# Kernel tuning notes

Hardware: AMD Instinct MI355X
Metric: run time of the kernel (lower is better)

Reference implementation:

```python
import jax, jax.numpy as jnp
import numpy as np

EMBED = 1024
HEADS = 16
HEAD_DIM = EMBED // HEADS


def setup_inputs() -> dict:
    key = jax.random.key(0)
    ks = jax.random.split(key, 5)
    s = 0.02
    x = jax.random.normal(ks[0], (2, 2048, EMBED), dtype=jnp.float32)
    W_qkv = jax.random.normal(ks[1], (EMBED, 3 * EMBED), dtype=jnp.float32) * s
    b_qkv = jnp.zeros((3 * EMBED,), dtype=jnp.float32)
    W_proj = jax.random.normal(ks[2], (EMBED, EMBED), dtype=jnp.float32) * s
    b_proj = jnp.zeros((EMBED,), dtype=jnp.float32)
    return {"x": x, "W_qkv": W_qkv, "b_qkv": b_qkv, "W_proj": W_proj, "b_proj": b_proj}


def reference(x, W_qkv, b_qkv, W_proj, b_proj):
    B, N, _ = x.shape
    scale = HEAD_DIM ** -0.5
    qkv = x @ W_qkv + b_qkv                     # [B,N,3E]
    qkv = qkv.reshape(B, N, 3, HEADS, HEAD_DIM)
    q = qkv[:, :, 0].transpose(0, 2, 1, 3) * scale  # [B,H,N,D]
    k = qkv[:, :, 1].transpose(0, 2, 1, 3)
    v = qkv[:, :, 2].transpose(0, 2, 1, 3)
    attn = jnp.einsum('bhnd,bhmd->bhnm', q, k)  # [B,H,N,N]
    attn = jax.nn.softmax(attn, axis=-1)
    out = jnp.einsum('bhnm,bhmd->bhnd', attn, v)  # [B,H,N,D]
    out = out.transpose(0, 2, 1, 3).reshape(B, N, HEADS * HEAD_DIM)
    return out @ W_proj + b_proj
```

## Files before the change

### kernel.cpp

```cpp
#include <hip/hip_runtime.h>
#include <hip/hip_bf16.h>
#include <stdint.h>

typedef unsigned short u16;
typedef __bf16 bf16x8 __attribute__((ext_vector_type(8)));
typedef float f32x4 __attribute__((ext_vector_type(4)));
typedef float f32x16 __attribute__((ext_vector_type(16)));

__device__ __forceinline__ u16 f2bf(float f) {
    union { float f; unsigned u; } x; x.f = f;
    unsigned u = x.u;
    u += 0x7FFFu + ((u >> 16) & 1u);
    return (u16)(u >> 16);
}
__device__ __forceinline__ float bf2f(u16 h) {
    union { unsigned u; float f; } x; x.u = ((unsigned)h) << 16; return x.f;
}

typedef __attribute__((address_space(1))) void gvoid;
typedef __attribute__((address_space(3))) void lvoid;
__device__ __forceinline__ void gl2lds16(const void* g, void* l) {
    __builtin_amdgcn_global_load_lds((gvoid*)g, (lvoid*)l, 16, 0, 0);
}

__global__ __launch_bounds__(256) void prep_kernel(
    const float* __restrict__ x, u16* __restrict__ xb,
    const float* __restrict__ Wqkv, u16* __restrict__ wqkvT,
    const float* __restrict__ Wproj, u16* __restrict__ wprojT)
{
    __shared__ u16 tile[64][65];
    const int blk = blockIdx.x;
    const int tid = threadIdx.x;

    if (blk < 2048) {
        const size_t i = ((size_t)blk * 256 + tid) * 8;
        float4 a = *(const float4*)(x + i);
        float4 b = *(const float4*)(x + i + 4);
        ushort4 oa, ob;
        oa.x = f2bf(a.x); oa.y = f2bf(a.y); oa.z = f2bf(a.z); oa.w = f2bf(a.w);
        ob.x = f2bf(b.x); ob.y = f2bf(b.y); ob.z = f2bf(b.z); ob.w = f2bf(b.w);
        *(ushort4*)(xb + i) = oa;
        *(ushort4*)(xb + i + 4) = ob;
        return;
    }
    const float* in; u16* out; int rows, cols, bx, by;
    if (blk < 2816) { int t = blk - 2048; in = Wqkv;  out = wqkvT;  rows = 1024; cols = 3072; bx = t % 48; by = t / 48; }
    else            { int t = blk - 2816; in = Wproj; out = wprojT; rows = 1024; cols = 1024; bx = t % 16; by = t / 16; }
#pragma unroll
    for (int i = 0; i < 16; i++) {
        int e = i * 256 + tid;
        int r = e >> 6, c = e & 63;
        tile[r][c] = f2bf(in[(size_t)(by * 64 + r) * cols + bx * 64 + c]);
    }
    __syncthreads();
#pragma unroll
    for (int i = 0; i < 16; i++) {
        int e = i * 256 + tid;
        int r = e >> 6, c = e & 63;
        out[(size_t)(bx * 64 + r) * rows + by * 64 + c] = tile[c][r];
    }
}

__global__ __launch_bounds__(256) void gemm_qkv(
    const u16* __restrict__ A, const u16* __restrict__ Bt,
    const float* __restrict__ bias,
    u16* __restrict__ q, u16* __restrict__ ko, u16* __restrict__ vt)
{
    constexpr int K = 1024;
    __shared__ __align__(16) u16 smem[64 * 64 + 128 * 64];
    u16* sA = smem;
    u16* sB = smem + 4096;
    const int tid = threadIdx.x;
    const int wave = tid >> 6, lane = tid & 63;
    const int quad = lane >> 4, l16 = lane & 15;
    const int wm = (wave >> 1) * 32, wn = (wave & 1) * 64;
    const int m0 = blockIdx.y * 64, n0 = blockIdx.x * 128;
    const int srow = lane >> 3;
    const int scolz = ((lane & 7) ^ srow) * 8;

    f32x4 acc[2][4];
#pragma unroll
    for (int i = 0; i < 2; i++)
#pragma unroll
        for (int j = 0; j < 4; j++)
#pragma unroll
            for (int r = 0; r < 4; r++) acc[i][j][r] = 0.f;

    for (int kt = 0; kt < K; kt += 64) {
        __syncthreads();
#pragma unroll
        for (int t = 0; t < 2; t++) {
            int rb = wave * 16 + t * 8;
            gl2lds16(A + (size_t)(m0 + rb + srow) * K + kt + scolz, &sA[rb * 64]);
        }
#pragma unroll
        for (int t = 0; t < 4; t++) {
            int rb = wave * 32 + t * 8;
            gl2lds16(Bt + (size_t)(n0 + rb + srow) * K + kt + scolz, &sB[rb * 64]);
        }
        __syncthreads();
#pragma unroll
        for (int kk = 0; kk < 64; kk += 32) {
            bf16x8 af[2], bfr[4];
            int sl = (((kk >> 3) + quad) ^ (l16 & 7)) * 8;
#pragma unroll
            for (int t = 0; t < 2; t++)
                af[t] = *(const bf16x8*)&sA[(wm + t * 16 + l16) * 64 + sl];
#pragma unroll
            for (int t = 0; t < 4; t++)
                bfr[t] = *(const bf16x8*)&sB[(wn + t * 16 + l16) * 64 + sl];
#pragma unroll
            for (int i = 0; i < 2; i++)
#pragma unroll
                for (int j = 0; j < 4; j++)
                    acc[i][j] = __builtin_amdgcn_mfma_f32_16x16x32_bf16(
                        af[i], bfr[j], acc[i][j], 0, 0, 0);
        }
    }

    const float QSCALE = 0.18033688011112042f;
    const float sc = (n0 < 1024) ? QSCALE : 1.0f;
    __syncthreads();
#pragma unroll
    for (int i = 0; i < 2; i++) {
#pragma unroll
        for (int j = 0; j < 4; j++) {
            float bv = bias[n0 + wn + j * 16 + l16];
#pragma unroll
            for (int r = 0; r < 4; r++) {
                float v = (acc[i][j][r] + bv) * sc;
                smem[(wm + i * 16 + quad * 4 + r) * 132 + wn + j * 16 + l16] = f2bf(v);
            }
        }
    }
    __syncthreads();

    if (n0 < 2048) {
        u16* dst = (n0 < 1024) ? q : ko;
#pragma unroll
        for (int it = 0; it < 4; it++) {
            int c = it * 256 + tid;
            int m_l = c >> 4;
            int n8 = (c & 15) * 8;
            uint4 w = *(const uint4*)&smem[m_l * 132 + n8];
            int n = n0 + n8;
            int h = (n & 1023) >> 6, d = n & 63;
            int m = m0 + m_l;
            int b = m >> 11, t = m & 2047;
            *(uint4*)(dst + ((size_t)(b * 16 + h) * 2048 + t) * 64 + d) = w;
        }
    } else {
        constexpr int PERM[16] = {0,1,2,3, 8,9,10,11, 4,5,6,7, 12,13,14,15};
        int nv = n0 - 2048;
        int n_l = tid & 127, mh = tid >> 7;
        int hh = (nv >> 6) + (n_l >> 6);
        int d = n_l & 63;
        int bb = m0 >> 11, t0 = m0 & 2047;
        u16* vrow = vt + ((size_t)(bb * 16 + hh) * 64 + d) * 2048 + t0 + mh * 32;
#pragma unroll
        for (int it = 0; it < 4; it++) {
            int base = mh * 32 + it * 8;
            union { u16 s[8]; uint4 w; } pk;
#pragma unroll
            for (int i = 0; i < 8; i++) {
                int pos = base + i;
                int row = (pos & ~15) | PERM[pos & 15];
                pk.s[i] = smem[row * 132 + n_l];
            }
            *(uint4*)(vrow + it * 8) = pk.w;
        }
    }
}

__global__ __launch_bounds__(256, 4) void attn_kernel(
    const u16* __restrict__ q, const u16* __restrict__ ko,
    const u16* __restrict__ vt,
    u16* __restrict__ op0, u16* __restrict__ op1,
    float* __restrict__ lp0, float* __restrict__ lp1)
{
    __shared__ __align__(16) u16 sK[2][64 * 72];
    __shared__ __align__(16) u16 sV[2][64 * 72];

    const int tid = threadIdx.x;
    const int wave = tid >> 6, lane = tid & 63;
    const int l31 = lane & 31, hi = lane >> 5;

    const int lid = blockIdx.x;
    const int xcd = lid & 7, idx = lid >> 3;
    const int h = xcd * 2 + (idx & 1);
    const int b = (idx >> 1) & 1;
    const int q0 = ((idx >> 2) & 15) * 128;
    const int khalf = idx >> 6;
    const int kbase = khalf * 1024;
    const size_t bh = (size_t)(b * 16 + h);

    const u16* qp  = q  + bh * 2048 * 64;
    const u16* kp  = ko + bh * 2048 * 64;
    const u16* vtp = vt + bh * 64 * 2048;

    bf16x8 qf[4];
    {
        const u16* qrow = qp + (size_t)(q0 + wave * 32 + l31) * 64 + hi * 8;
#pragma unroll
        for (int d = 0; d < 4; d++)
            qf[d] = *(const bf16x8*)(qrow + d * 16);
    }

    const int sr0 = tid >> 3;
    const int sc0 = (tid & 7) * 8;
    const int sr1 = sr0 + 32;

    uint4 pk0 = *(const uint4*)(kp + (size_t)(kbase + sr0) * 64 + sc0);
    uint4 pk1 = *(const uint4*)(kp + (size_t)(kbase + sr1) * 64 + sc0);
    uint4 pv0 = *(const uint4*)(vtp + (size_t)sr0 * 2048 + kbase + sc0);
    uint4 pv1 = *(const uint4*)(vtp + (size_t)sr1 * 2048 + kbase + sc0);

    f32x16 accO[2];
#pragma unroll
    for (int d = 0; d < 2; d++)
#pragma unroll
        for (int r = 0; r < 16; r++) accO[d][r] = 0.f;
    float ls[4] = {0.f, 0.f, 0.f, 0.f};

    for (int t = 0; t < 16; ++t) {
        const int cur = t & 1;
        u16* sKc = &sK[cur][0];
        u16* sVc = &sV[cur][0];
        *(uint4*)&sKc[sr0 * 72 + sc0] = pk0;
        *(uint4*)&sKc[sr1 * 72 + sc0] = pk1;
        *(uint4*)&sVc[sr0 * 72 + sc0] = pv0;
        *(uint4*)&sVc[sr1 * 72 + sc0] = pv1;
        if (t < 15) {
            int nt = kbase + (t + 1) * 64;
            pk0 = *(const uint4*)(kp + (size_t)(nt + sr0) * 64 + sc0);
            pk1 = *(const uint4*)(kp + (size_t)(nt + sr1) * 64 + sc0);
            pv0 = *(const uint4*)(vtp + (size_t)sr0 * 2048 + nt + sc0);
            pv1 = *(const uint4*)(vtp + (size_t)sr1 * 2048 + nt + sc0);
        }
        __syncthreads();

#pragma unroll
        for (int rb = 0; rb < 2; rb++) {
            f32x16 S;
#pragma unroll
            for (int r = 0; r < 16; r++) S[r] = 0.f;
            const u16* krd = &sKc[(rb * 32 + l31) * 72 + hi * 8];
#pragma unroll
            for (int d = 0; d < 4; d++) {
                bf16x8 kf = *(const bf16x8*)(krd + d * 16);
                S = __builtin_amdgcn_mfma_f32_32x32x16_bf16(kf, qf[d], S, 0, 0, 0);
            }
            union { float f; unsigned u; } e[16];
#pragma unroll
            for (int r = 0; r < 16; r++) {
                e[r].f = __builtin_amdgcn_exp2f(S[r]);
                ls[r & 3] += e[r].f;
            }
#pragma unroll
            for (int ks2 = 0; ks2 < 2; ks2++) {
                union { unsigned u[4]; bf16x8 v; } pa;
#pragma unroll
                for (int s = 0; s < 4; s++) {
                    unsigned r0 = e[ks2 * 8 + 2 * s].u + 0x8000u;
                    unsigned r1 = e[ks2 * 8 + 2 * s + 1].u + 0x8000u;
                    pa.u[s] = (r1 & 0xFFFF0000u) | (r0 >> 16);
                }
                const int nb = rb * 32 + ks2 * 16 + hi * 8;
#pragma unroll
                for (int db = 0; db < 2; db++) {
                    bf16x8 vf = *(const bf16x8*)&sVc[(db * 32 + l31) * 72 + nb];
                    accO[db] = __builtin_amdgcn_mfma_f32_32x32x16_bf16(pa.v, vf, accO[db], 0, 0, 0);
                }
            }
        }
    }

    u16* op = khalf ? op1 : op0;
    float* lp = khalf ? lp1 : lp0;

    float lsum = (ls[0] + ls[1]) + (ls[2] + ls[3]);
    float ltot = lsum + __shfl_xor(lsum, 32, 64);
    int qq0 = q0 + wave * 32;
    if (hi == 0) lp[bh * 2048 + qq0 + l31] = ltot;

#pragma unroll
    for (int db = 0; db < 2; db++)
#pragma unroll
        for (int r = 0; r < 16; r++) {
            int tq = qq0 + (r & 3) + 8 * (r >> 2) + 4 * hi;
            size_t row = (size_t)b * 2048 + tq;
            op[row * 1024 + h * 64 + db * 32 + l31] = f2bf(accO[db][r]);
        }
}

__global__ __launch_bounds__(256) void combine_kernel(
    const u16* __restrict__ op0, const u16* __restrict__ op1,
    const float* __restrict__ lp0, const float* __restrict__ lp1,
    u16* __restrict__ ob)
{
    const size_t i = ((size_t)blockIdx.x * 256 + threadIdx.x) * 8;
    int m = (int)(i >> 10), e = (int)(i & 1023);
    int b = m >> 11, t = m & 2047, h = e >> 6;
    float inv = 1.f / (lp0[(size_t)(b * 16 + h) * 2048 + t] +
                       lp1[(size_t)(b * 16 + h) * 2048 + t]);
    union { uint4 w; u16 s[8]; } a, c, o;
    a.w = *(const uint4*)(op0 + i);
    c.w = *(const uint4*)(op1 + i);
#pragma unroll
    for (int k = 0; k < 8; k++)
        o.s[k] = f2bf((bf2f(a.s[k]) + bf2f(c.s[k])) * inv);
    *(uint4*)(ob + i) = o.w;
}

__global__ __launch_bounds__(256) void gemm_proj(
    const u16* __restrict__ A, const u16* __restrict__ Bt,
    const float* __restrict__ bias, float* __restrict__ out)
{
    constexpr int K = 1024;
    __shared__ __align__(16) u16 sA[64 * 64];
    __shared__ __align__(16) u16 sB[128 * 64];
    const int tid = threadIdx.x;
    const int wave = tid >> 6, lane = tid & 63;
    const int quad = lane >> 4, l16 = lane & 15;
    const int wm = (wave & 1) * 32, wn = (wave >> 1) * 64;

    const int lid = blockIdx.x;
    const int xcd = lid & 7, idx = lid >> 3;
    const int m0 = (xcd * 8 + (idx & 7)) * 64;
    const int n0 = (idx >> 3) * 128;

    const int srow = lane >> 3;
    const int scolz = ((lane & 7) ^ srow) * 8;

    f32x4 acc[2][4];
#pragma unroll
    for (int i = 0; i < 2; i++)
#pragma unroll
        for (int j = 0; j < 4; j++)
#pragma unroll
            for (int r = 0; r < 4; r++) acc[i][j][r] = 0.f;

    for (int kt = 0; kt < K; kt += 64) {
        __syncthreads();
#pragma unroll
        for (int t = 0; t < 2; t++) {
            int rb = wave * 16 + t * 8;
            gl2lds16(A + (size_t)(m0 + rb + srow) * K + kt + scolz, &sA[rb * 64]);
        }
#pragma unroll
        for (int t = 0; t < 4; t++) {
            int rb = wave * 32 + t * 8;
            gl2lds16(Bt + (size_t)(n0 + rb + srow) * K + kt + scolz, &sB[rb * 64]);
        }
        __syncthreads();
#pragma unroll
        for (int kk = 0; kk < 64; kk += 32) {
            bf16x8 af[2], bfr[4];
            int sl = (((kk >> 3) + quad) ^ (l16 & 7)) * 8;
#pragma unroll
            for (int t = 0; t < 2; t++)
                af[t] = *(const bf16x8*)&sA[(wm + t * 16 + l16) * 64 + sl];
#pragma unroll
            for (int t = 0; t < 4; t++)
                bfr[t] = *(const bf16x8*)&sB[(wn + t * 16 + l16) * 64 + sl];
#pragma unroll
            for (int i = 0; i < 2; i++)
#pragma unroll
                for (int j = 0; j < 4; j++)
                    acc[i][j] = __builtin_amdgcn_mfma_f32_16x16x32_bf16(
                        af[i], bfr[j], acc[i][j], 0, 0, 0);
        }
    }

#pragma unroll
    for (int i = 0; i < 2; i++) {
#pragma unroll
        for (int j = 0; j < 4; j++) {
            int n = n0 + wn + j * 16 + l16;
            float bv = bias[n];
#pragma unroll
            for (int r = 0; r < 4; r++) {
                int m = m0 + wm + i * 16 + quad * 4 + r;
                out[(size_t)m * 1024 + n] = acc[i][j][r] + bv;
            }
        }
    }
}

extern "C" void kernel_launch(void* const* d_in, const int* in_sizes, int n_in,
                              void* d_out, int out_size, void* d_ws, size_t ws_size,
                              hipStream_t stream) {
    const float* x     = (const float*)d_in[0];
    const float* Wqkv  = (const float*)d_in[1];
    const float* bqkv  = (const float*)d_in[2];
    const float* Wproj = (const float*)d_in[3];
    const float* bproj = (const float*)d_in[4];
    float* out = (float*)d_out;
    char* ws = (char*)d_ws;

    u16* wqkvT  = (u16*)(ws);
    u16* wprojT = (u16*)(ws +  6291456);
    u16* xb     = (u16*)(ws +  8388608);
    u16* qb     = (u16*)(ws + 16777216);
    u16* kb     = (u16*)(ws + 25165824);
    u16* vtb    = (u16*)(ws + 33554432);
    u16* ob     = (u16*)(ws + 41943040);

    u16*   op0 = ob;
    u16*   op1 = xb;
    float* lp0 = (float*)wqkvT;
    float* lp1 = (float*)(ws + 262144);

    prep_kernel<<<dim3(3072), 256, 0, stream>>>(x, xb, Wqkv, wqkvT, Wproj, wprojT);
    gemm_qkv<<<dim3(24, 64), 256, 0, stream>>>(xb, wqkvT, bqkv, qb, kb, vtb);
    attn_kernel<<<dim3(1024), 256, 0, stream>>>(qb, kb, vtb, op0, op1, lp0, lp1);
    combine_kernel<<<dim3(2048), 256, 0, stream>>>(op0, op1, lp0, lp1, ob);
    gemm_proj<<<dim3(512), 256, 0, stream>>>(ob, wprojT, bproj, out);
}
```

Measured before the change: 189.6 us.

## Merge attention key-split halves in-block and shrink projection GEMM tiles

The attention kernel now runs both key halves inside one 512-thread block, with waves 4-7 taking the second half. The partial outputs and row sums are combined through shared memory, which removes the separate combine kernel and its global round trip of partial outputs. Separately, the projection GEMM moves to 32x128 tiles with twice as many blocks, to improve occupancy and tail balance. The trade-offs are fewer, larger attention blocks with double the LDS per block, and less data reuse per projection tile.

```diff
diff --git a/kernel.cpp b/kernel.cpp
--- a/kernel.cpp
+++ b/kernel.cpp
@@ -172,26 +172,24 @@
     }
 }
 
-__global__ __launch_bounds__(256, 4) void attn_kernel(
+__global__ __launch_bounds__(512) void attn_kernel(
     const u16* __restrict__ q, const u16* __restrict__ ko,
-    const u16* __restrict__ vt,
-    u16* __restrict__ op0, u16* __restrict__ op1,
-    float* __restrict__ lp0, float* __restrict__ lp1)
+    const u16* __restrict__ vt, u16* __restrict__ ob)
 {
-    __shared__ __align__(16) u16 sK[2][64 * 72];
-    __shared__ __align__(16) u16 sV[2][64 * 72];
+    __shared__ __align__(16) u16 sK[2][2][64 * 72];
+    __shared__ __align__(16) u16 sV[2][2][64 * 72];
 
     const int tid = threadIdx.x;
     const int wave = tid >> 6, lane = tid & 63;
     const int l31 = lane & 31, hi = lane >> 5;
+    const int khalf = wave >> 2, qw = wave & 3;
+    const int kbase = khalf * 1024;
 
     const int lid = blockIdx.x;
     const int xcd = lid & 7, idx = lid >> 3;
     const int h = xcd * 2 + (idx & 1);
     const int b = (idx >> 1) & 1;
     const int q0 = ((idx >> 2) & 15) * 128;
-    const int khalf = idx >> 6;
-    const int kbase = khalf * 1024;
     const size_t bh = (size_t)(b * 16 + h);
 
     const u16* qp  = q  + bh * 2048 * 64;
@@ -200,14 +198,15 @@
 
     bf16x8 qf[4];
     {
-        const u16* qrow = qp + (size_t)(q0 + wave * 32 + l31) * 64 + hi * 8;
+        const u16* qrow = qp + (size_t)(q0 + qw * 32 + l31) * 64 + hi * 8;
 #pragma unroll
         for (int d = 0; d < 4; d++)
             qf[d] = *(const bf16x8*)(qrow + d * 16);
     }
 
-    const int sr0 = tid >> 3;
-    const int sc0 = (tid & 7) * 8;
+    const int gt = tid & 255;
+    const int sr0 = gt >> 3;
+    const int sc0 = (gt & 7) * 8;
     const int sr1 = sr0 + 32;
 
     uint4 pk0 = *(const uint4*)(kp + (size_t)(kbase + sr0) * 64 + sc0);
@@ -224,8 +223,8 @@
 
     for (int t = 0; t < 16; ++t) {
         const int cur = t & 1;
-        u16* sKc = &sK[cur][0];
-        u16* sVc = &sV[cur][0];
+        u16* sKc = &sK[khalf][cur][0];
+        u16* sVc = &sV[khalf][cur][0];
         *(uint4*)&sKc[sr0 * 72 + sc0] = pk0;
         *(uint4*)&sKc[sr1 * 72 + sc0] = pk1;
         *(uint4*)&sVc[sr0 * 72 + sc0] = pv0;
@@ -275,41 +274,36 @@
         }
     }
 
-    u16* op = khalf ? op1 : op0;
-    float* lp = khalf ? lp1 : lp0;
-
     float lsum = (ls[0] + ls[1]) + (ls[2] + ls[3]);
     float ltot = lsum + __shfl_xor(lsum, 32, 64);
-    int qq0 = q0 + wave * 32;
-    if (hi == 0) lp[bh * 2048 + qq0 + l31] = ltot;
-
-#pragma unroll
-    for (int db = 0; db < 2; db++)
-#pragma unroll
-        for (int r = 0; r < 16; r++) {
-            int tq = qq0 + (r & 3) + 8 * (r >> 2) + 4 * hi;
-            size_t row = (size_t)b * 2048 + tq;
-            op[row * 1024 + h * 64 + db * 32 + l31] = f2bf(accO[db][r]);
-        }
-}
-
-__global__ __launch_bounds__(256) void combine_kernel(
-    const u16* __restrict__ op0, const u16* __restrict__ op1,
-    const float* __restrict__ lp0, const float* __restrict__ lp1,
-    u16* __restrict__ ob)
-{
-    const size_t i = ((size_t)blockIdx.x * 256 + threadIdx.x) * 8;
-    int m = (int)(i >> 10), e = (int)(i & 1023);
-    int b = m >> 11, t = m & 2047, h = e >> 6;
-    float inv = 1.f / (lp0[(size_t)(b * 16 + h) * 2048 + t] +
-                       lp1[(size_t)(b * 16 + h) * 2048 + t]);
-    union { uint4 w; u16 s[8]; } a, c, o;
-    a.w = *(const uint4*)(op0 + i);
-    c.w = *(const uint4*)(op1 + i);
-#pragma unroll
-    for (int k = 0; k < 8; k++)
-        o.s[k] = f2bf((bf2f(a.s[k]) + bf2f(c.s[k])) * inv);
-    *(uint4*)(ob + i) = o.w;
+
+    float* xO = (float*)&sK[0][0][0];
+    float* xL = (float*)&sV[0][0][0];
+
+    __syncthreads();
+    if (hi == 0) xL[khalf * 128 + qw * 32 + l31] = ltot;
+    if (khalf == 1) {
+#pragma unroll
+        for (int db = 0; db < 2; db++)
+#pragma unroll
+            for (int r = 0; r < 16; r++) {
+                int rloc = (r & 3) + 8 * (r >> 2) + 4 * hi;
+                xO[(qw * 32 + rloc) * 64 + db * 32 + l31] = accO[db][r];
+            }
+    }
+    __syncthreads();
+    if (khalf == 0) {
+#pragma unroll
+        for (int db = 0; db < 2; db++)
+#pragma unroll
+            for (int r = 0; r < 16; r++) {
+                int rloc = (r & 3) + 8 * (r >> 2) + 4 * hi;
+                float inv = 1.f / (xL[qw * 32 + rloc] + xL[128 + qw * 32 + rloc]);
+                float v = (accO[db][r] + xO[(qw * 32 + rloc) * 64 + db * 32 + l31]) * inv;
+                int tq = q0 + qw * 32 + rloc;
+                ob[((size_t)b * 2048 + tq) * 1024 + h * 64 + db * 32 + l31] = f2bf(v);
+            }
+    }
 }
 
 __global__ __launch_bounds__(256) void gemm_proj(
@@ -317,34 +311,33 @@
     const float* __restrict__ bias, float* __restrict__ out)
 {
     constexpr int K = 1024;
-    __shared__ __align__(16) u16 sA[64 * 64];
+    __shared__ __align__(16) u16 sA[32 * 64];
     __shared__ __align__(16) u16 sB[128 * 64];
     const int tid = threadIdx.x;
     const int wave = tid >> 6, lane = tid & 63;
     const int quad = lane >> 4, l16 = lane & 15;
-    const int wm = (wave & 1) * 32, wn = (wave >> 1) * 64;
+    const int wn = wave * 32;
 
     const int lid = blockIdx.x;
     const int xcd = lid & 7, idx = lid >> 3;
-    const int m0 = (xcd * 8 + (idx & 7)) * 64;
-    const int n0 = (idx >> 3) * 128;
+    const int m0 = (xcd * 16 + (idx & 15)) * 32;
+    const int n0 = (idx >> 4) * 128;
 
     const int srow = lane >> 3;
     const int scolz = ((lane & 7) ^ srow) * 8;
 
-    f32x4 acc[2][4];
+    f32x4 acc[2][2];
 #pragma unroll
     for (int i = 0; i < 2; i++)
 #pragma unroll
-        for (int j = 0; j < 4; j++)
+        for (int j = 0; j < 2; j++)
 #pragma unroll
             for (int r = 0; r < 4; r++) acc[i][j][r] = 0.f;
 
     for (int kt = 0; kt < K; kt += 64) {
         __syncthreads();
-#pragma unroll
-        for (int t = 0; t < 2; t++) {
-            int rb = wave * 16 + t * 8;
+        {
+            int rb = wave * 8;
             gl2lds16(A + (size_t)(m0 + rb + srow) * K + kt + scolz, &sA[rb * 64]);
         }
 #pragma unroll
@@ -355,18 +348,18 @@
         __syncthreads();
 #pragma unroll
         for (int kk = 0; kk < 64; kk += 32) {
-            bf16x8 af[2], bfr[4];
+            bf16x8 af[2], bfr[2];
             int sl = (((kk >> 3) + quad) ^ (l16 & 7)) * 8;
 #pragma unroll
             for (int t = 0; t < 2; t++)
-                af[t] = *(const bf16x8*)&sA[(wm + t * 16 + l16) * 64 + sl];
-#pragma unroll
-            for (int t = 0; t < 4; t++)
+                af[t] = *(const bf16x8*)&sA[(t * 16 + l16) * 64 + sl];
+#pragma unroll
+            for (int t = 0; t < 2; t++)
                 bfr[t] = *(const bf16x8*)&sB[(wn + t * 16 + l16) * 64 + sl];
 #pragma unroll
             for (int i = 0; i < 2; i++)
 #pragma unroll
-                for (int j = 0; j < 4; j++)
+                for (int j = 0; j < 2; j++)
                     acc[i][j] = __builtin_amdgcn_mfma_f32_16x16x32_bf16(
                         af[i], bfr[j], acc[i][j], 0, 0, 0);
         }
@@ -375,12 +368,12 @@
 #pragma unroll
     for (int i = 0; i < 2; i++) {
 #pragma unroll
-        for (int j = 0; j < 4; j++) {
+        for (int j = 0; j < 2; j++) {
             int n = n0 + wn + j * 16 + l16;
             float bv = bias[n];
 #pragma unroll
             for (int r = 0; r < 4; r++) {
-                int m = m0 + wm + i * 16 + quad * 4 + r;
+                int m = m0 + i * 16 + quad * 4 + r;
                 out[(size_t)m * 1024 + n] = acc[i][j][r] + bv;
             }
         }
@@ -406,14 +399,8 @@
     u16* vtb    = (u16*)(ws + 33554432);
     u16* ob     = (u16*)(ws + 41943040);
 
-    u16*   op0 = ob;
-    u16*   op1 = xb;
-    float* lp0 = (float*)wqkvT;
-    float* lp1 = (float*)(ws + 262144);
-
     prep_kernel<<<dim3(3072), 256, 0, stream>>>(x, xb, Wqkv, wqkvT, Wproj, wprojT);
     gemm_qkv<<<dim3(24, 64), 256, 0, stream>>>(xb, wqkvT, bqkv, qb, kb, vtb);
-    attn_kernel<<<dim3(1024), 256, 0, stream>>>(qb, kb, vtb, op0, op1, lp0, lp1);
-    combine_kernel<<<dim3(2048), 256, 0, stream>>>(op0, op1, lp0, lp1, ob);
-    gemm_proj<<<dim3(512), 256, 0, stream>>>(ob, wprojT, bproj, out);
-}
+    attn_kernel<<<dim3(512), 512, 0, stream>>>(qb, kb, vtb, ob);
+    gemm_proj<<<dim3(1024), 256, 0, stream>>>(ob, wprojT, bproj, out);
+}
```

New measurement: 178.8 us. -5.7%, faster.

## Fuse split-K attention combine into projection GEMM A-tile load

Applied to the files above, without the earlier changes.

Removes the separate combine kernel. The projection GEMM now loads both partial attention outputs and their row sums directly, normalizes them, and writes the bf16 result into shared memory as its A tile. This avoids writing and re-reading the combined intermediate buffer and saves one kernel launch. In exchange the A load becomes a synchronous register path instead of a direct global-to-LDS load, the normalization is redone for every N-block, and the block tile is shrunk to 32 rows with twice as many blocks, which lowers data reuse per block.

```diff
diff --git a/kernel.cpp b/kernel.cpp
--- a/kernel.cpp
+++ b/kernel.cpp
@@ -293,59 +293,53 @@
         }
 }
 
-__global__ __launch_bounds__(256) void combine_kernel(
+__global__ __launch_bounds__(256) void gemm_proj(
     const u16* __restrict__ op0, const u16* __restrict__ op1,
     const float* __restrict__ lp0, const float* __restrict__ lp1,
-    u16* __restrict__ ob)
-{
-    const size_t i = ((size_t)blockIdx.x * 256 + threadIdx.x) * 8;
-    int m = (int)(i >> 10), e = (int)(i & 1023);
-    int b = m >> 11, t = m & 2047, h = e >> 6;
-    float inv = 1.f / (lp0[(size_t)(b * 16 + h) * 2048 + t] +
-                       lp1[(size_t)(b * 16 + h) * 2048 + t]);
-    union { uint4 w; u16 s[8]; } a, c, o;
-    a.w = *(const uint4*)(op0 + i);
-    c.w = *(const uint4*)(op1 + i);
-#pragma unroll
-    for (int k = 0; k < 8; k++)
-        o.s[k] = f2bf((bf2f(a.s[k]) + bf2f(c.s[k])) * inv);
-    *(uint4*)(ob + i) = o.w;
-}
-
-__global__ __launch_bounds__(256) void gemm_proj(
-    const u16* __restrict__ A, const u16* __restrict__ Bt,
+    const u16* __restrict__ Bt,
     const float* __restrict__ bias, float* __restrict__ out)
 {
     constexpr int K = 1024;
-    __shared__ __align__(16) u16 sA[64 * 64];
+    __shared__ __align__(16) u16 sA[32 * 64];
     __shared__ __align__(16) u16 sB[128 * 64];
     const int tid = threadIdx.x;
     const int wave = tid >> 6, lane = tid & 63;
     const int quad = lane >> 4, l16 = lane & 15;
-    const int wm = (wave & 1) * 32, wn = (wave >> 1) * 64;
+    const int wn = wave * 32;
 
     const int lid = blockIdx.x;
     const int xcd = lid & 7, idx = lid >> 3;
-    const int m0 = (xcd * 8 + (idx & 7)) * 64;
-    const int n0 = (idx >> 3) * 128;
+    const int m0 = (xcd * 16 + (idx & 15)) * 32;
+    const int n0 = (idx >> 4) * 128;
 
     const int srow = lane >> 3;
     const int scolz = ((lane & 7) ^ srow) * 8;
 
-    f32x4 acc[2][4];
+    f32x4 acc[2][2];
 #pragma unroll
     for (int i = 0; i < 2; i++)
 #pragma unroll
-        for (int j = 0; j < 4; j++)
+        for (int j = 0; j < 2; j++)
 #pragma unroll
             for (int r = 0; r < 4; r++) acc[i][j][r] = 0.f;
 
     for (int kt = 0; kt < K; kt += 64) {
         __syncthreads();
-#pragma unroll
-        for (int t = 0; t < 2; t++) {
-            int rb = wave * 16 + t * 8;
-            gl2lds16(A + (size_t)(m0 + rb + srow) * K + kt + scolz, &sA[rb * 64]);
+        {
+            int rb = wave * 8;
+            int m = m0 + rb + srow;
+            int hh = kt >> 6;
+            int tt = m & 2047, bb = m >> 11;
+            size_t li = ((size_t)(bb * 16 + hh)) * 2048 + tt;
+            float inv = 1.f / (lp0[li] + lp1[li]);
+            size_t off = (size_t)m * K + kt + scolz;
+            union { uint4 w; u16 s[8]; } x0, x1, xo;
+            x0.w = *(const uint4*)(op0 + off);
+            x1.w = *(const uint4*)(op1 + off);
+#pragma unroll
+            for (int s = 0; s < 8; s++)
+                xo.s[s] = f2bf((bf2f(x0.s[s]) + bf2f(x1.s[s])) * inv);
+            *(uint4*)&sA[rb * 64 + lane * 8] = xo.w;
         }
 #pragma unroll
         for (int t = 0; t < 4; t++) {
@@ -355,18 +349,18 @@
         __syncthreads();
 #pragma unroll
         for (int kk = 0; kk < 64; kk += 32) {
-            bf16x8 af[2], bfr[4];
+            bf16x8 af[2], bfr[2];
             int sl = (((kk >> 3) + quad) ^ (l16 & 7)) * 8;
 #pragma unroll
             for (int t = 0; t < 2; t++)
-                af[t] = *(const bf16x8*)&sA[(wm + t * 16 + l16) * 64 + sl];
-#pragma unroll
-            for (int t = 0; t < 4; t++)
+                af[t] = *(const bf16x8*)&sA[(t * 16 + l16) * 64 + sl];
+#pragma unroll
+            for (int t = 0; t < 2; t++)
                 bfr[t] = *(const bf16x8*)&sB[(wn + t * 16 + l16) * 64 + sl];
 #pragma unroll
             for (int i = 0; i < 2; i++)
 #pragma unroll
-                for (int j = 0; j < 4; j++)
+                for (int j = 0; j < 2; j++)
                     acc[i][j] = __builtin_amdgcn_mfma_f32_16x16x32_bf16(
                         af[i], bfr[j], acc[i][j], 0, 0, 0);
         }
@@ -375,12 +369,12 @@
 #pragma unroll
     for (int i = 0; i < 2; i++) {
 #pragma unroll
-        for (int j = 0; j < 4; j++) {
+        for (int j = 0; j < 2; j++) {
             int n = n0 + wn + j * 16 + l16;
             float bv = bias[n];
 #pragma unroll
             for (int r = 0; r < 4; r++) {
-                int m = m0 + wm + i * 16 + quad * 4 + r;
+                int m = m0 + i * 16 + quad * 4 + r;
                 out[(size_t)m * 1024 + n] = acc[i][j][r] + bv;
             }
         }
@@ -404,9 +398,9 @@
     u16* qb     = (u16*)(ws + 16777216);
     u16* kb     = (u16*)(ws + 25165824);
     u16* vtb    = (u16*)(ws + 33554432);
-    u16* ob     = (u16*)(ws + 41943040);
-
-    u16*   op0 = ob;
+    u16* obuf   = (u16*)(ws + 41943040);
+
+    u16*   op0 = obuf;
     u16*   op1 = xb;
     float* lp0 = (float*)wqkvT;
     float* lp1 = (float*)(ws + 262144);
@@ -414,6 +408,5 @@
     prep_kernel<<<dim3(3072), 256, 0, stream>>>(x, xb, Wqkv, wqkvT, Wproj, wprojT);
     gemm_qkv<<<dim3(24, 64), 256, 0, stream>>>(xb, wqkvT, bqkv, qb, kb, vtb);
     attn_kernel<<<dim3(1024), 256, 0, stream>>>(qb, kb, vtb, op0, op1, lp0, lp1);
-    combine_kernel<<<dim3(2048), 256, 0, stream>>>(op0, op1, lp0, lp1, ob);
-    gemm_proj<<<dim3(512), 256, 0, stream>>>(ob, wprojT, bproj, out);
-}
+    gemm_proj<<<dim3(1024), 256, 0, stream>>>(op0, op1, lp0, lp1, wprojT, bproj, out);
+}
```

Result: faster. 183.0 us (-3.4%).
